# Performance work log

Hardware: AMD Instinct MI355X
Metric: run time of the kernel (lower is better)

The kernel has to match this reference:

```python
import jax, jax.numpy as jnp
import numpy as np
import math

N0 = 50000      # nodes at level 0
E0 = 800000     # edges at level 0 (fixed edge buffer, masked when pooled)
D = 128         # hidden_dim == latent_dim
L = 2           # args.mpl_layers
NB = 2          # args.num_blocks (SAGEConvs per block)
RATIO = 0.5     # args.mpl_ratio
EPS = 1e-12


def setup_inputs() -> dict:
    key = jax.random.key(0)
    ks = jax.random.split(key, 6)
    x = jax.random.normal(ks[0], (N0, D), jnp.float32)
    edge_index = jax.random.randint(ks[1], (2, E0), 0, N0, jnp.int32)
    n_convs = (2 * L + 1) * NB  # down(4) + bottom(2) + up(4) = 10
    Wl = jax.random.normal(ks[2], (n_convs, D, D), jnp.float32) * 0.05
    bl = jax.random.normal(ks[3], (n_convs, D), jnp.float32) * 0.05
    Wr = jax.random.normal(ks[4], (n_convs, D, D), jnp.float32) * 0.05
    pool_p = jax.random.normal(ks[5], (L, D), jnp.float32)
    return {"x": x, "edge_index": edge_index, "Wl": Wl, "bl": bl, "Wr": Wr,
            "pool_p": pool_p}


def _sage(x, src, dst, valid, W_l, b_l, W_r, n):
    """PyG SAGEConv (mean aggr): lin_l(mean_{j->i} x_j) + lin_r(x_i).
    Invalid (masked) edges contribute neither to the sum nor the count."""
    msg = x[src] * valid[:, None]                       # [E, D]
    s = jax.ops.segment_sum(msg, dst, num_segments=n)   # [n, D]
    cnt = jax.ops.segment_sum(valid, dst, num_segments=n)
    mean = s / jnp.maximum(cnt, 1.0)[:, None]
    return mean @ W_l.T + b_l + x @ W_r.T


def _cal_ew(w, src, dst, valid, n):
    """WeightedEdgeConv.cal_ew (no_grad in original)."""
    deg = jax.ops.segment_sum(valid, src, num_segments=n)
    normed = w / jnp.where(deg > 0, deg, 1.0)
    w_send = normed[src] * valid
    aggr_w = jax.ops.segment_sum(w_send, dst, num_segments=n) + EPS
    ec = w_send / aggr_w[dst]
    return jax.lax.stop_gradient(ec), jax.lax.stop_gradient(aggr_w)


def _econv(x, src, dst, ec, n, aggregating=True):
    """WeightedEdgeConv.forward: gather -> scale by edge weight -> scatter-add."""
    if aggregating:
        return jax.ops.segment_sum(x[src] * ec[:, None], dst, num_segments=n)
    return jax.ops.segment_sum(x[dst] * ec[:, None], src, num_segments=n)


def reference(x, edge_index, Wl, bl, Wr, pool_p):
    src, dst = edge_index[0], edge_index[1]
    valid = jnp.ones((E0,), x.dtype)
    n = N0
    conv = 0
    down_outs, down_edges, ecs, perms, sizes = [], [], [], [], []
    w = jnp.ones((N0,), x.dtype)  # b_data.weights (ones by default)

    # ---- down path ----
    for l in range(L):
        for _ in range(NB):
            x = _sage(x, src, dst, valid, Wl[conv], bl[conv], Wr[conv], n)
            conv += 1
        down_outs.append(x)
        down_edges.append((src, dst, valid))
        sizes.append(n)
        ec, w = _cal_ew(w, src, dst, valid, n)
        ecs.append(ec)
        x = _econv(x, src, dst, ec, n, aggregating=True)
        # TopKPooling: score = x.p/||p||, keep top ceil(ratio*n), gate by tanh
        p = pool_p[l]
        score = x @ p / jnp.linalg.norm(p)
        k = int(math.ceil(RATIO * n))
        vals, perm = jax.lax.top_k(score, k)
        x = x[perm] * jnp.tanh(vals)[:, None]
        w = w[perm]
        new_id = jnp.full((n,), -1, jnp.int32).at[perm].set(
            jnp.arange(k, dtype=jnp.int32))
        src2, dst2 = new_id[src], new_id[dst]
        keep = ((src2 >= 0) & (dst2 >= 0)).astype(x.dtype)
        valid = valid * keep
        src = jnp.maximum(src2, 0)
        dst = jnp.maximum(dst2, 0)
        perms.append(perm)
        n = k

    # ---- bottom ----
    for _ in range(NB):
        x = _sage(x, src, dst, valid, Wl[conv], bl[conv], Wr[conv], n)
        conv += 1

    # ---- up path ----
    for i in range(L):
        u = L - 1 - i
        src, dst, valid = down_edges[u]
        n = sizes[u]
        # Unpool: scatter into zeros at kept-node indices
        x = jnp.zeros((n, x.shape[-1]), x.dtype).at[perms[u]].set(x)
        x = _econv(x, src, dst, ecs[u], n, aggregating=False)
        for _ in range(NB):
            x = _sage(x, src, dst, valid, Wl[conv], bl[conv], Wr[conv], n)
            conv += 1
        x = x + down_outs[u]  # skip connection
    return x
```

## Files before the change

### kernel.cpp

```cpp
#include <hip/hip_runtime.h>
#include <stdint.h>

#define DEV __device__ __forceinline__

constexpr int N0 = 50000;
constexpr int E0 = 800000;
constexpr int D  = 128;

typedef __attribute__((ext_vector_type(8))) short bf16x8;
typedef __attribute__((ext_vector_type(4))) float f32x4;

DEV float bf2f(unsigned u) { return __uint_as_float(u << 16); }
DEV unsigned short f2bf(float f) {
  unsigned u = __float_as_uint(f);
  unsigned r = u + 0x7fffu + ((u >> 16) & 1u);
  return (unsigned short)(r >> 16);
}

DEV unsigned wave_incl_scan(unsigned v, int lane) {
  #pragma unroll
  for (int off = 1; off < 64; off <<= 1) {
    unsigned u = __shfl_up(v, (unsigned)off);
    if (lane >= off) v += u;
  }
  return v;
}

__global__ void k_count(const int* __restrict__ src, const int* __restrict__ dst,
                        unsigned* cnt_src, unsigned* cnt_dst,
                        unsigned* __restrict__ rank_src, unsigned* __restrict__ rank_dst) {
  int e = blockIdx.x * blockDim.x + threadIdx.x;
  if (e < E0) {
    rank_src[e] = atomicAdd(&cnt_src[src[e]], 1u);
    rank_dst[e] = atomicAdd(&cnt_dst[dst[e]], 1u);
  }
}

__global__ void k_psum2(const unsigned* __restrict__ in0, const unsigned* __restrict__ in1,
                        int n, unsigned* __restrict__ part) {
  int y = blockIdx.y;
  const unsigned* in = y ? in1 : in0;
  int t = threadIdx.x, lane = t & 63, w = t >> 6;
  int base = blockIdx.x * 1024 + t * 4;
  unsigned s = 0;
  #pragma unroll
  for (int j = 0; j < 4; ++j) { int i = base + j; if (i < n) s += in[i]; }
  #pragma unroll
  for (int off = 32; off >= 1; off >>= 1) s += __shfl_xor(s, off);
  __shared__ unsigned ws[4];
  if (lane == 0) ws[w] = s;
  __syncthreads();
  if (t == 0) part[y * 64 + blockIdx.x] = ws[0] + ws[1] + ws[2] + ws[3];
}

__global__ void k_sapply2(const unsigned* __restrict__ in0, const unsigned* __restrict__ in1,
                          const unsigned* __restrict__ part, int n, int nch,
                          unsigned* __restrict__ out0, unsigned* __restrict__ out1) {
  int y = blockIdx.y;
  const unsigned* in = y ? in1 : in0;
  unsigned* out = y ? out1 : out0;
  int t = threadIdx.x, lane = t & 63, w = t >> 6;
  unsigned c = (lane < (int)blockIdx.x) ? part[y * 64 + lane] : 0u;
  #pragma unroll
  for (int off = 32; off >= 1; off >>= 1) c += __shfl_xor(c, off);
  int base = blockIdx.x * 1024 + t * 4;
  unsigned v[4]; unsigned s = 0;
  #pragma unroll
  for (int j = 0; j < 4; ++j) { int i = base + j; v[j] = (i < n) ? in[i] : 0u; s += v[j]; }
  unsigned incl = wave_incl_scan(s, lane);
  __shared__ unsigned wsum[4], woff[4];
  if (lane == 63) wsum[w] = incl;
  __syncthreads();
  if (t == 0) { unsigned run = 0; for (int j = 0; j < 4; ++j) { woff[j] = run; run += wsum[j]; } }
  __syncthreads();
  unsigned run = c + woff[w] + incl - s;
  #pragma unroll
  for (int j = 0; j < 4; ++j) {
    int i = base + j;
    if (i < n) out[i] = run;
    run += v[j];
  }
  if ((int)blockIdx.x == nch - 1 && t == 0)
    out[n] = c + woff[3] + wsum[3];
}

__global__ void k_fill2(const int* __restrict__ src, const int* __restrict__ dst,
                        const unsigned* __restrict__ rank_src, const unsigned* __restrict__ rank_dst,
                        const unsigned* __restrict__ indptr_src, const unsigned* __restrict__ indptr_dst,
                        int* __restrict__ adj_src, int* __restrict__ adj_dst) {
  int e = blockIdx.x * blockDim.x + threadIdx.x;
  if (e < E0) {
    int s = src[e], d = dst[e];
    adj_dst[indptr_dst[d] + rank_dst[e]] = s;
    adj_src[indptr_src[s] + rank_src[e]] = d;
  }
}

__global__ void k_adj_next2(const int* __restrict__ adjd, const int* __restrict__ adjs,
                            const int* __restrict__ new_id,
                            int* __restrict__ outd, int* __restrict__ outs) {
  int pos = blockIdx.x * blockDim.x + threadIdx.x;
  if (pos < E0) {
    int a = adjd[pos];
    outd[pos] = (a >= 0) ? new_id[a] : -1;
    int b = adjs[pos];
    outs[pos] = (b >= 0) ? new_id[b] : -1;
  }
}

__global__ void k_adj_next(const int* __restrict__ adj_prev, const int* __restrict__ new_id,
                           int* __restrict__ adj_out) {
  int pos = blockIdx.x * blockDim.x + threadIdx.x;
  if (pos < E0) {
    int a = adj_prev[pos];
    adj_out[pos] = (a >= 0) ? new_id[a] : -1;
  }
}

__global__ void k_wt_pk3(const float* __restrict__ Wl, const float* __restrict__ Wr,
                         unsigned short* __restrict__ Bh, unsigned short* __restrict__ Bm,
                         unsigned short* __restrict__ Bl) {
  int idx = blockIdx.x * blockDim.x + threadIdx.x;
  if (idx >= 10 * 8 * 8 * 64) return;
  int l  = idx & 63;
  int ct = (idx >> 6) & 7;
  int ks = (idx >> 9) & 7;
  int c  = idx >> 12;
  int k0 = ks * 32 + (l >> 4) * 8;
  int o  = ct * 16 + (l & 15);
  const float* Wrow = (k0 < 128) ? (Wl + ((size_t)c * 128 + o) * 128 + k0)
                                 : (Wr + ((size_t)c * 128 + o) * 128 + (k0 - 128));
  size_t base = (size_t)idx * 8;
  #pragma unroll
  for (int j = 0; j < 8; ++j) {
    float wv = Wrow[j];
    unsigned short h = f2bf(wv);
    float r1 = wv - bf2f(h);
    unsigned short m = f2bf(r1);
    float r2 = r1 - bf2f(m);
    Bh[base + j] = h;
    Bm[base + j] = m;
    Bl[base + j] = f2bf(r2);
  }
}

template<bool MEAN, bool MASKED, bool ECW>
__global__ void k_gf32(const float* __restrict__ x, const int* __restrict__ adj,
                       const float* __restrict__ ecs, const unsigned* __restrict__ indptr,
                       const int* __restrict__ orig, int n, float* __restrict__ out) {
  int wid = (blockIdx.x * blockDim.x + threadIdx.x) >> 6;
  int lane = threadIdx.x & 63;
  if (wid >= n) return;
  int o = orig ? orig[wid] : wid;
  unsigned s0 = indptr[o], s1 = indptr[o + 1];
  int q = lane >> 4, sl = lane & 15;
  float acc[8];
  #pragma unroll
  for (int k = 0; k < 8; ++k) acc[k] = 0.f;
  float cnt = 0.f;
  for (unsigned idx = s0; idx < s1; idx += 16) {
    #pragma unroll
    for (int j = 0; j < 4; ++j) {
      unsigned e = idx + j * 4 + q;
      if (e < s1) {
        int a = adj[e];
        if (!MASKED || a >= 0) {
          const float4 v0 = *(const float4*)(x + (size_t)a * D + sl * 8);
          const float4 v1 = *(const float4*)(x + (size_t)a * D + sl * 8 + 4);
          if (ECW) {
            float w = ecs[e];
            acc[0] = fmaf(w, v0.x, acc[0]); acc[1] = fmaf(w, v0.y, acc[1]);
            acc[2] = fmaf(w, v0.z, acc[2]); acc[3] = fmaf(w, v0.w, acc[3]);
            acc[4] = fmaf(w, v1.x, acc[4]); acc[5] = fmaf(w, v1.y, acc[5]);
            acc[6] = fmaf(w, v1.z, acc[6]); acc[7] = fmaf(w, v1.w, acc[7]);
          } else {
            acc[0] += v0.x; acc[1] += v0.y; acc[2] += v0.z; acc[3] += v0.w;
            acc[4] += v1.x; acc[5] += v1.y; acc[6] += v1.z; acc[7] += v1.w;
          }
          cnt += 1.f;
        }
      }
    }
  }
  #pragma unroll
  for (int k = 0; k < 8; ++k) {
    acc[k] += __shfl_xor(acc[k], 16);
    acc[k] += __shfl_xor(acc[k], 32);
  }
  if (MEAN) {
    cnt += __shfl_xor(cnt, 16);
    cnt += __shfl_xor(cnt, 32);
    if (!MASKED) cnt = (float)(s1 - s0);
    float inv = 1.0f / fmaxf(cnt, 1.0f);
    #pragma unroll
    for (int k = 0; k < 8; ++k) acc[k] *= inv;
  }
  if (q == 0) {
    *(float4*)(out + (size_t)wid * D + sl * 8)     = make_float4(acc[0], acc[1], acc[2], acc[3]);
    *(float4*)(out + (size_t)wid * D + sl * 8 + 4) = make_float4(acc[4], acc[5], acc[6], acc[7]);
  }
}

template<bool MEAN, bool MASKED, bool ECW>
__global__ void k_gbf(const unsigned* __restrict__ xb, const int* __restrict__ adj,
                      const float* __restrict__ ecs, const unsigned* __restrict__ indptr,
                      const int* __restrict__ orig, int n,
                      float* __restrict__ out, unsigned* __restrict__ outbf) {
  int wid = (blockIdx.x * blockDim.x + threadIdx.x) >> 6;
  int lane = threadIdx.x & 63;
  if (wid >= n) return;
  int o = orig ? orig[wid] : wid;
  unsigned s0 = indptr[o], s1 = indptr[o + 1];
  int q = lane >> 4, sl = lane & 15;
  float acc[8];
  #pragma unroll
  for (int k = 0; k < 8; ++k) acc[k] = 0.f;
  float cnt = 0.f;
  for (unsigned idx = s0; idx < s1; idx += 16) {
    #pragma unroll
    for (int j = 0; j < 4; ++j) {
      unsigned e = idx + j * 4 + q;
      if (e < s1) {
        int a = adj[e];
        if (!MASKED || a >= 0) {
          const uint4 v = *(const uint4*)(xb + (size_t)a * 64 + sl * 4);
          float f0 = bf2f(v.x & 0xffffu), f1 = bf2f(v.x >> 16);
          float f2 = bf2f(v.y & 0xffffu), f3 = bf2f(v.y >> 16);
          float f4 = bf2f(v.z & 0xffffu), f5 = bf2f(v.z >> 16);
          float f6 = bf2f(v.w & 0xffffu), f7 = bf2f(v.w >> 16);
          if (ECW) {
            float w = ecs[e];
            acc[0] = fmaf(w, f0, acc[0]); acc[1] = fmaf(w, f1, acc[1]);
            acc[2] = fmaf(w, f2, acc[2]); acc[3] = fmaf(w, f3, acc[3]);
            acc[4] = fmaf(w, f4, acc[4]); acc[5] = fmaf(w, f5, acc[5]);
            acc[6] = fmaf(w, f6, acc[6]); acc[7] = fmaf(w, f7, acc[7]);
          } else {
            acc[0] += f0; acc[1] += f1; acc[2] += f2; acc[3] += f3;
            acc[4] += f4; acc[5] += f5; acc[6] += f6; acc[7] += f7;
          }
          cnt += 1.f;
        }
      }
    }
  }
  #pragma unroll
  for (int k = 0; k < 8; ++k) {
    acc[k] += __shfl_xor(acc[k], 16);
    acc[k] += __shfl_xor(acc[k], 32);
  }
  if (MEAN) {
    cnt += __shfl_xor(cnt, 16);
    cnt += __shfl_xor(cnt, 32);
    if (!MASKED) cnt = (float)(s1 - s0);
    float inv = 1.0f / fmaxf(cnt, 1.0f);
    #pragma unroll
    for (int k = 0; k < 8; ++k) acc[k] *= inv;
  }
  if (q == 0) {
    *(float4*)(out + (size_t)wid * D + sl * 8)     = make_float4(acc[0], acc[1], acc[2], acc[3]);
    *(float4*)(out + (size_t)wid * D + sl * 8 + 4) = make_float4(acc[4], acc[5], acc[6], acc[7]);
    if (outbf) {
      uint4 p;
      p.x = (unsigned)f2bf(acc[0]) | ((unsigned)f2bf(acc[1]) << 16);
      p.y = (unsigned)f2bf(acc[2]) | ((unsigned)f2bf(acc[3]) << 16);
      p.z = (unsigned)f2bf(acc[4]) | ((unsigned)f2bf(acc[5]) << 16);
      p.w = (unsigned)f2bf(acc[6]) | ((unsigned)f2bf(acc[7]) << 16);
      *(uint4*)(outbf + (size_t)wid * 64 + sl * 4) = p;
    }
  }
}

__launch_bounds__(256)
__global__ void k_gemm_mfma6(const float* __restrict__ mean, const float* __restrict__ xin,
                             const unsigned short* __restrict__ Bh, const unsigned short* __restrict__ Bm,
                             const unsigned short* __restrict__ Bl,
                             const float* __restrict__ bias,
                             float* __restrict__ y, int n) {
  int tid = threadIdx.x;
  int lane = tid & 63, w = tid >> 6;
  int row0 = blockIdx.x * 64 + w * 16;
  int arow = row0 + (lane & 15);
  int kgrp = lane >> 4;
  bool rowok = arow < n;
  f32x4 acc[8];
  #pragma unroll
  for (int ct = 0; ct < 8; ++ct) acc[ct] = f32x4{0.f, 0.f, 0.f, 0.f};

  #pragma unroll
  for (int ks = 0; ks < 8; ++ks) {
    const float* A = (ks < 4) ? mean : xin;
    int kk = (ks & 3) * 32 + kgrp * 8;
    float av[8];
    if (rowok) {
      float4 x0 = *(const float4*)(A + (size_t)arow * D + kk);
      float4 x1 = *(const float4*)(A + (size_t)arow * D + kk + 4);
      av[0] = x0.x; av[1] = x0.y; av[2] = x0.z; av[3] = x0.w;
      av[4] = x1.x; av[5] = x1.y; av[6] = x1.z; av[7] = x1.w;
    } else {
      #pragma unroll
      for (int j = 0; j < 8; ++j) av[j] = 0.f;
    }
    bf16x8 ah, am, al;
    #pragma unroll
    for (int j = 0; j < 8; ++j) {
      unsigned short h = f2bf(av[j]);
      float r1 = av[j] - bf2f(h);
      unsigned short m = f2bf(r1);
      float r2 = r1 - bf2f(m);
      ah[j] = (short)h; am[j] = (short)m; al[j] = (short)f2bf(r2);
    }
    #pragma unroll
    for (int ct = 0; ct < 8; ++ct) {
      size_t boff = (((size_t)ks * 8 + ct) * 64 + lane) * 8;
      bf16x8 bh = *(const bf16x8*)(Bh + boff);
      bf16x8 bm = *(const bf16x8*)(Bm + boff);
      bf16x8 bl = *(const bf16x8*)(Bl + boff);
      acc[ct] = __builtin_amdgcn_mfma_f32_16x16x32_bf16(ah, bh, acc[ct], 0, 0, 0);
      acc[ct] = __builtin_amdgcn_mfma_f32_16x16x32_bf16(ah, bm, acc[ct], 0, 0, 0);
      acc[ct] = __builtin_amdgcn_mfma_f32_16x16x32_bf16(am, bh, acc[ct], 0, 0, 0);
      acc[ct] = __builtin_amdgcn_mfma_f32_16x16x32_bf16(am, bm, acc[ct], 0, 0, 0);
      acc[ct] = __builtin_amdgcn_mfma_f32_16x16x32_bf16(ah, bl, acc[ct], 0, 0, 0);
      acc[ct] = __builtin_amdgcn_mfma_f32_16x16x32_bf16(al, bh, acc[ct], 0, 0, 0);
    }
  }
  int ccol = lane & 15;
  #pragma unroll
  for (int ct = 0; ct < 8; ++ct) {
    int col = ct * 16 + ccol;
    float bb = bias[col];
    #pragma unroll
    for (int r = 0; r < 4; ++r) {
      int row = row0 + kgrp * 4 + r;
      if (row < n) y[(size_t)row * D + col] = acc[ct][r] + bb;
    }
  }
}

__launch_bounds__(256)
__global__ void k_gemm_mfma(const float* __restrict__ mean, const float* __restrict__ xin,
                            const unsigned short* __restrict__ Bhi, const unsigned short* __restrict__ Blo,
                            const float* __restrict__ bias, const float* __restrict__ skip,
                            float* __restrict__ y, unsigned short* __restrict__ ybf, int n) {
  int tid = threadIdx.x;
  int lane = tid & 63, w = tid >> 6;
  int row0 = blockIdx.x * 64 + w * 16;
  int arow = row0 + (lane & 15);
  int kgrp = lane >> 4;
  bool rowok = arow < n;
  f32x4 acc[8];
  #pragma unroll
  for (int ct = 0; ct < 8; ++ct) acc[ct] = f32x4{0.f, 0.f, 0.f, 0.f};

  #pragma unroll
  for (int ks = 0; ks < 8; ++ks) {
    const float* A = (ks < 4) ? mean : xin;
    int kk = (ks & 3) * 32 + kgrp * 8;
    float av[8];
    if (rowok) {
      float4 x0 = *(const float4*)(A + (size_t)arow * D + kk);
      float4 x1 = *(const float4*)(A + (size_t)arow * D + kk + 4);
      av[0] = x0.x; av[1] = x0.y; av[2] = x0.z; av[3] = x0.w;
      av[4] = x1.x; av[5] = x1.y; av[6] = x1.z; av[7] = x1.w;
    } else {
      #pragma unroll
      for (int j = 0; j < 8; ++j) av[j] = 0.f;
    }
    bf16x8 ahi, alo;
    #pragma unroll
    for (int j = 0; j < 8; ++j) {
      unsigned short h = f2bf(av[j]);
      ahi[j] = (short)h;
      alo[j] = (short)f2bf(av[j] - bf2f(h));
    }
    #pragma unroll
    for (int ct = 0; ct < 8; ++ct) {
      size_t boff = (((size_t)ks * 8 + ct) * 64 + lane) * 8;
      bf16x8 bh = *(const bf16x8*)(Bhi + boff);
      bf16x8 bl = *(const bf16x8*)(Blo + boff);
      acc[ct] = __builtin_amdgcn_mfma_f32_16x16x32_bf16(ahi, bh, acc[ct], 0, 0, 0);
      acc[ct] = __builtin_amdgcn_mfma_f32_16x16x32_bf16(alo, bh, acc[ct], 0, 0, 0);
      acc[ct] = __builtin_amdgcn_mfma_f32_16x16x32_bf16(ahi, bl, acc[ct], 0, 0, 0);
    }
  }
  int ccol = lane & 15;
  #pragma unroll
  for (int ct = 0; ct < 8; ++ct) {
    int col = ct * 16 + ccol;
    float bb = bias[col];
    #pragma unroll
    for (int r = 0; r < 4; ++r) {
      int row = row0 + kgrp * 4 + r;
      if (row < n) {
        float v = acc[ct][r] + bb;
        if (skip) v += skip[(size_t)row * D + col];
        y[(size_t)row * D + col] = v;
        if (ybf) ybf[(size_t)row * D + col] = f2bf(v);
      }
    }
  }
}

__global__ void k_deg_mask(const int* __restrict__ adj_src, const unsigned* __restrict__ indptr_src,
                           const int* __restrict__ orig, int n, float* __restrict__ deg) {
  int j = blockIdx.x * blockDim.x + threadIdx.x;
  if (j >= n) return;
  int o = orig ? orig[j] : j;
  unsigned s0 = indptr_src[o], s1 = indptr_src[o + 1];
  float d = 0.f;
  for (unsigned i = s0; i < s1; ++i) d += (adj_src[i] >= 0) ? 1.f : 0.f;
  deg[j] = d;
}

template<bool MASKED>
__global__ void k_ew_dst(const int* __restrict__ adj, const unsigned* __restrict__ indptr,
                         const unsigned* __restrict__ ips,
                         const int* __restrict__ orig, const float* __restrict__ w,
                         const float* __restrict__ deg, int n,
                         float* __restrict__ ws_slot, float* __restrict__ aggrw,
                         float* __restrict__ ec_slot) {
  int j = blockIdx.x * blockDim.x + threadIdx.x;
  if (j >= n) return;
  int o = orig ? orig[j] : j;
  unsigned s0 = indptr[o], s1 = indptr[o + 1];
  float s = 1e-12f;
  for (unsigned pos = s0; pos < s1; ++pos) {
    int a = adj[pos];
    float ws = 0.f;
    if (!MASKED || a >= 0) {
      float d = deg ? deg[a] : (float)(ips[a + 1] - ips[a]);
      ws = (w ? w[a] : 1.0f) / (d > 0.f ? d : 1.0f);
    }
    ws_slot[pos] = ws;
    s += ws;
  }
  aggrw[j] = s;
  float inv = 1.0f / s;
  for (unsigned pos = s0; pos < s1; ++pos) ec_slot[pos] = ws_slot[pos] * inv;
}

template<bool MASKED>
__global__ void k_ew_src(const int* __restrict__ adj_src, const unsigned* __restrict__ indptr_src,
                         const int* __restrict__ orig, const float* __restrict__ w,
                         const float* __restrict__ deg, const float* __restrict__ aggrw, int n,
                         float* __restrict__ ec_slot) {
  int j = blockIdx.x * blockDim.x + threadIdx.x;
  if (j >= n) return;
  int o = orig ? orig[j] : j;
  unsigned s0 = indptr_src[o], s1 = indptr_src[o + 1];
  float d = deg ? deg[j] : (float)(s1 - s0);
  float wn = (w ? w[j] : 1.0f) / (d > 0.f ? d : 1.0f);
  for (unsigned pos = s0; pos < s1; ++pos) {
    int a = adj_src[pos];
    ec_slot[pos] = (!MASKED || a >= 0) ? (wn / aggrw[a]) : 0.f;
  }
}

DEV unsigned mono_key(float f) {
  unsigned u = __float_as_uint(f);
  return (u & 0x80000000u) ? ~u : (u | 0x80000000u);
}

__global__ void k_score(const float* __restrict__ x, const float* __restrict__ p,
                        int n, float* __restrict__ score, unsigned* __restrict__ keys,
                        unsigned* bins, unsigned* state, int k) {
  if (blockIdx.x == 0) {
    int t = threadIdx.x;
    if (t < 256) bins[t] = 0u;
    if (t == 0) { state[0] = 0u; state[1] = (unsigned)k; }
  }
  int wid = (blockIdx.x * blockDim.x + threadIdx.x) >> 6;
  int lane = threadIdx.x & 63;
  if (wid >= n) return;
  float p0 = p[lane * 2], p1 = p[lane * 2 + 1];
  const float2 xv = *(const float2*)(x + (size_t)wid * D + lane * 2);
  float partial = xv.x * p0 + xv.y * p1;
  float pn = p0 * p0 + p1 * p1;
  #pragma unroll
  for (int off = 32; off >= 1; off >>= 1) {
    partial += __shfl_xor(partial, off);
    pn += __shfl_xor(pn, off);
  }
  if (lane == 0) {
    float sc = partial * (1.0f / sqrtf(pn));
    score[wid] = sc;
    keys[wid] = mono_key(sc);
  }
}

__global__ void k_hist(const unsigned* __restrict__ keys, int n, const unsigned* __restrict__ state,
                       unsigned* __restrict__ bins, int byte) {
  __shared__ unsigned lb[256];
  for (int i = threadIdx.x; i < 256; i += blockDim.x) lb[i] = 0u;
  __syncthreads();
  unsigned prefix = state[0];
  unsigned mask = (byte == 3) ? 0u : (0xFFFFFFFFu << ((byte + 1) * 8));
  for (int i = blockIdx.x * blockDim.x + threadIdx.x; i < n; i += gridDim.x * blockDim.x) {
    unsigned key = keys[i];
    if ((key & mask) == (prefix & mask))
      atomicAdd(&lb[(key >> (byte * 8)) & 255], 1u);
  }
  __syncthreads();
  for (int i = threadIdx.x; i < 256; i += blockDim.x)
    if (lb[i]) atomicAdd(&bins[i], lb[i]);
}

__global__ void k_pick(unsigned* bins, unsigned* state, int byte) {
  if (threadIdx.x == 0) {
    unsigned r = state[1];
    int b;
    for (b = 255; b > 0; --b) {
      unsigned c = bins[b];
      if (c >= r) break;
      r -= c;
    }
    state[0] |= ((unsigned)b) << (byte * 8);
    state[1] = r;
  }
  __syncthreads();
  for (int i = threadIdx.x; i < 256; i += blockDim.x) bins[i] = 0u;
}

__global__ void k_flags(const unsigned* __restrict__ keys, const unsigned* __restrict__ state,
                        int n, uint2* __restrict__ part) {
  int t = threadIdx.x, lane = t & 63, w = t >> 6;
  int base = blockIdx.x * 1024 + t * 4;
  unsigned T = state[0];
  unsigned cnt = 0;
  #pragma unroll
  for (int j = 0; j < 4; ++j) {
    int i = base + j;
    if (i < n) {
      unsigned key = keys[i];
      cnt += (key > T ? 1u : 0u) + ((key == T ? 1u : 0u) << 16);
    }
  }
  #pragma unroll
  for (int off = 32; off >= 1; off >>= 1) cnt += __shfl_xor(cnt, off);
  __shared__ unsigned ws[4];
  if (lane == 0) ws[w] = cnt;
  __syncthreads();
  if (t == 0) {
    unsigned s = ws[0] + ws[1] + ws[2] + ws[3];
    part[blockIdx.x] = make_uint2(s & 0xffffu, s >> 16);
  }
}

__global__ void k_pack2(const unsigned* __restrict__ keys, const unsigned* __restrict__ state,
                        const uint2* __restrict__ part, const float* __restrict__ aggrw,
                        const int* __restrict__ orig, int n,
                        int* __restrict__ perm, int* __restrict__ new_id,
                        float* __restrict__ w_next, int* __restrict__ orig_next) {
  int t = threadIdx.x, lane = t & 63, w = t >> 6;
  int base = blockIdx.x * 1024 + t * 4;
  unsigned T = state[0], r = state[1];
  unsigned co = 0;
  if (lane < (int)blockIdx.x) {
    uint2 pp = part[lane];
    co = pp.x | (pp.y << 16);
  }
  #pragma unroll
  for (int off = 32; off >= 1; off >>= 1) co += __shfl_xor(co, off);
  unsigned f[4];
  unsigned cnt = 0;
  #pragma unroll
  for (int j = 0; j < 4; ++j) {
    int i = base + j;
    unsigned key = (i < n) ? keys[i] : 0u;
    unsigned gt = (i < n && key > T) ? 1u : 0u;
    unsigned eq = (i < n && key == T) ? 1u : 0u;
    f[j] = gt | (eq << 1);
    cnt += gt + (eq << 16);
  }
  unsigned incl = wave_incl_scan(cnt, lane);
  __shared__ unsigned wsum[4], woff[4];
  if (lane == 63) wsum[w] = incl;
  __syncthreads();
  if (t == 0) { unsigned run = 0; for (int j = 0; j < 4; ++j) { woff[j] = run; run += wsum[j]; } }
  __syncthreads();
  unsigned before = woff[w] + incl - cnt;
  unsigned gt_b = (co & 0xffffu) + (before & 0xffffu);
  unsigned eq_b = (co >> 16) + (before >> 16);
  #pragma unroll
  for (int j = 0; j < 4; ++j) {
    int i = base + j;
    if (i >= n) break;
    unsigned gt = f[j] & 1u, eq = (f[j] >> 1) & 1u;
    bool sel = gt || (eq && eq_b < r);
    if (sel) {
      int pos = (int)(gt_b + (eq_b < r ? eq_b : r));
      perm[pos] = i;
      new_id[i] = pos;
      w_next[pos] = aggrw[i];
      orig_next[pos] = orig ? orig[i] : i;
    } else {
      new_id[i] = -1;
    }
    gt_b += gt; eq_b += eq;
  }
}

__global__ void k_gate(const float* __restrict__ xin, const int* __restrict__ perm,
                       const float* __restrict__ score, int k, float* __restrict__ xout,
                       unsigned* __restrict__ outbf) {
  int wid = (blockIdx.x * blockDim.x + threadIdx.x) >> 6;
  int lane = threadIdx.x & 63;
  if (wid >= k) return;
  int j = perm[wid];
  float g = tanhf(score[j]);
  float2 v = *(const float2*)(xin + (size_t)j * D + lane * 2);
  v.x *= g; v.y *= g;
  *(float2*)(xout + (size_t)wid * D + lane * 2) = v;
  if (outbf) {
    unsigned p = (unsigned)f2bf(v.x) | ((unsigned)f2bf(v.y) << 16);
    outbf[(size_t)wid * 64 + lane] = p;
  }
}

__global__ void k_unpool_bf(const float* __restrict__ xin, const int* __restrict__ new_id,
                            int n, unsigned* __restrict__ outbf) {
  int wid = (blockIdx.x * blockDim.x + threadIdx.x) >> 6;
  int lane = threadIdx.x & 63;
  if (wid >= n) return;
  int j = new_id[wid];
  unsigned pk = 0u;
  if (j >= 0) {
    float2 v = *(const float2*)(xin + (size_t)j * D + lane * 2);
    pk = (unsigned)f2bf(v.x) | ((unsigned)f2bf(v.y) << 16);
  }
  outbf[(size_t)wid * 64 + lane] = pk;
}

extern "C" void kernel_launch(void* const* d_in, const int* in_sizes, int n_in,
                              void* d_out, int out_size, void* d_ws, size_t ws_size,
                              hipStream_t stream) {
  const float* x_in   = (const float*)d_in[0];
  const int*   ei     = (const int*)d_in[1];
  const int*   src0   = ei;
  const int*   dst0   = ei + E0;
  const float* Wl     = (const float*)d_in[2];
  const float* bl     = (const float*)d_in[3];
  const float* Wr     = (const float*)d_in[4];
  const float* pool_p = (const float*)d_in[5];
  float* out = (float*)d_out;

  const int n0 = N0, k0 = 25000, n1 = 25000, k1 = 12500, n2 = 12500;
  const int NCH0 = (N0 + 1023) / 1024;

  char* ws = (char*)d_ws;
  size_t off = 0;
  auto alloc = [&](size_t bytes) -> char* {
    char* p = ws + off;
    off += (bytes + 255) & ~(size_t)255;
    return p;
  };
  const size_t NBY = (size_t)N0 * D * 4;
  float* B0    = (float*)alloc(NBY);
  float* B1    = (float*)alloc(NBY);
  float* B2    = (float*)alloc(NBY);
  float* down0 = (float*)alloc(NBY);
  float* down1 = (float*)alloc(NBY / 2);
  unsigned* MA = (unsigned*)alloc((size_t)N0 * D * 2);
  unsigned* MB = (unsigned*)alloc((size_t)N0 * D * 2);
  int* adj0_dst = (int*)alloc(E0 * 4);
  int* adj0_src = (int*)alloc(E0 * 4);
  int* adj1_dst = (int*)alloc(E0 * 4);
  int* adj1_src = (int*)alloc(E0 * 4);
  float* ec0_src = (float*)alloc(E0 * 4);
  float* ec1_src = (float*)alloc(E0 * 4);
  float* ec_dst  = (float*)alloc(E0 * 4);
  float* ws_slot = (float*)alloc(E0 * 4);
  int* adj2_dst  = (int*)ws_slot;
  unsigned* rank_src = (unsigned*)alloc(E0 * 4);
  unsigned* rank_dst = (unsigned*)alloc(E0 * 4);
  unsigned* indptr_dst = (unsigned*)alloc((N0 + 1) * 4);
  unsigned* indptr_src = (unsigned*)alloc((N0 + 1) * 4);
  unsigned* cnt_src = (unsigned*)alloc(N0 * 4);
  unsigned* cnt_dst = (unsigned*)alloc(N0 * 4);
  float* deg   = (float*)alloc(N0 * 4);
  float* aggrw = (float*)alloc(N0 * 4);
  float* w1 = (float*)alloc(n1 * 4);
  float* w2 = (float*)alloc(n2 * 4);
  float* score = (float*)alloc(N0 * 4);
  unsigned* keys = (unsigned*)alloc(N0 * 4);
  int* perm0 = (int*)alloc(k0 * 4);
  int* perm1 = (int*)alloc(k1 * 4);
  int* orig1 = (int*)alloc(k0 * 4);
  int* orig2 = (int*)alloc(k1 * 4);
  int* new_id0 = (int*)alloc(N0 * 4);
  int* new_id1 = (int*)alloc(N0 * 4);
  unsigned* bins  = (unsigned*)alloc(256 * 4);
  unsigned* state = (unsigned*)alloc(8);
  unsigned* spart = (unsigned*)alloc(128 * 4);
  uint2* ppart = (uint2*)alloc(64 * 8);
  unsigned short* Bh = (unsigned short*)alloc((size_t)10 * 32768 * 2);
  unsigned short* Bm = (unsigned short*)alloc((size_t)10 * 32768 * 2);
  unsigned short* Bl = (unsigned short*)alloc((size_t)10 * 32768 * 2);

  const int EG = (E0 + 255) / 256;

  hipMemsetAsync(cnt_src, 0, N0 * 4, stream);
  hipMemsetAsync(cnt_dst, 0, N0 * 4, stream);
  k_count<<<EG, 256, 0, stream>>>(src0, dst0, cnt_src, cnt_dst, rank_src, rank_dst);
  k_psum2<<<dim3(NCH0, 2), 256, 0, stream>>>(cnt_src, cnt_dst, N0, spart);
  k_sapply2<<<dim3(NCH0, 2), 256, 0, stream>>>(cnt_src, cnt_dst, spart, N0, NCH0,
                                               indptr_src, indptr_dst);
  k_fill2<<<EG, 256, 0, stream>>>(src0, dst0, rank_src, rank_dst, indptr_src, indptr_dst,
                                  adj0_src, adj0_dst);
  k_wt_pk3<<<(10 * 8 * 8 * 64 + 255) / 256, 256, 0, stream>>>(Wl, Wr, Bh, Bm, Bl);

  auto gemm6 = [&](const float* meanb, const float* xin, float* yout, int n, int cidx) {
    size_t o = (size_t)cidx * 32768;
    k_gemm_mfma6<<<(n + 63) / 64, 256, 0, stream>>>(meanb, xin, Bh + o, Bm + o, Bl + o,
                                                    bl + cidx * 128, yout, n);
  };
  auto gemm_mx = [&](const float* meanb, const float* xin, float* yout, unsigned short* ybf,
                     const float* skip, int n, int cidx) {
    size_t o = (size_t)cidx * 32768;
    k_gemm_mfma<<<(n + 63) / 64, 256, 0, stream>>>(meanb, xin, Bh + o, Bm + o,
                                                   bl + cidx * 128, skip, yout, ybf, n);
  };

  auto pool_sel = [&](const float* xpool, int n, int kk, int level, const int* orig,
                      int* perm, int* nid, float* w_next, int* orig_next,
                      float* xout, unsigned* xout_bf) {
    int nch = (n + 1023) / 1024;
    k_score<<<(n + 3) / 4, 256, 0, stream>>>(xpool, pool_p + level * D, n, score, keys,
                                             bins, state, kk);
    for (int byte = 3; byte >= 0; --byte) {
      k_hist<<<256, 256, 0, stream>>>(keys, n, state, bins, byte);
      k_pick<<<1, 256, 0, stream>>>(bins, state, byte);
    }
    k_flags<<<nch, 256, 0, stream>>>(keys, state, n, ppart);
    k_pack2<<<nch, 256, 0, stream>>>(keys, state, ppart, aggrw, orig, n, perm, nid, w_next, orig_next);
    k_gate<<<(kk + 3) / 4, 256, 0, stream>>>(xpool, perm, score, kk, xout, xout_bf);
  };

  const int G0 = (n0 + 3) / 4, G1 = (n1 + 3) / 4, G2 = (n2 + 3) / 4;

  k_gf32<true, false, false><<<G0, 256, 0, stream>>>(x_in, adj0_dst, nullptr, indptr_dst, nullptr, n0, B1);
  gemm6(B1, x_in, B2, n0, 0);
  k_gf32<true, false, false><<<G0, 256, 0, stream>>>(B2, adj0_dst, nullptr, indptr_dst, nullptr, n0, B1);
  gemm6(B1, B2, down0, n0, 1);
  k_ew_dst<false><<<(n0 + 255) / 256, 256, 0, stream>>>(adj0_dst, indptr_dst, indptr_src, nullptr,
                                                        nullptr, nullptr, n0, ws_slot, aggrw, ec_dst);
  k_ew_src<false><<<(n0 + 255) / 256, 256, 0, stream>>>(adj0_src, indptr_src, nullptr, nullptr,
                                                        nullptr, aggrw, n0, ec0_src);
  k_gf32<false, false, true><<<G0, 256, 0, stream>>>(down0, adj0_dst, ec_dst, indptr_dst, nullptr, n0, B1);
  pool_sel(B1, n0, k0, 0, nullptr, perm0, new_id0, w1, orig1, B2, nullptr);
  k_adj_next2<<<EG, 256, 0, stream>>>(adj0_dst, adj0_src, new_id0, adj1_dst, adj1_src);

  k_gf32<true, true, false><<<G1, 256, 0, stream>>>(B2, adj1_dst, nullptr, indptr_dst, orig1, n1, B1);
  gemm6(B1, B2, B0, n1, 2);
  k_gf32<true, true, false><<<G1, 256, 0, stream>>>(B0, adj1_dst, nullptr, indptr_dst, orig1, n1, B1);
  gemm6(B1, B0, down1, n1, 3);
  k_deg_mask<<<(n1 + 255) / 256, 256, 0, stream>>>(adj1_src, indptr_src, orig1, n1, deg);
  k_ew_dst<true><<<(n1 + 255) / 256, 256, 0, stream>>>(adj1_dst, indptr_dst, nullptr, orig1, w1,
                                                       deg, n1, ws_slot, aggrw, ec_dst);
  k_ew_src<true><<<(n1 + 255) / 256, 256, 0, stream>>>(adj1_src, indptr_src, orig1, w1, deg, aggrw,
                                                       n1, ec1_src);
  k_gf32<false, true, true><<<G1, 256, 0, stream>>>(down1, adj1_dst, ec_dst, indptr_dst, orig1, n1, B1);
  pool_sel(B1, n1, k1, 1, orig1, perm1, new_id1, w2, orig2, B2, MA);
  k_adj_next<<<EG, 256, 0, stream>>>(adj1_dst, new_id1, adj2_dst);

  k_gbf<true, true, false><<<G2, 256, 0, stream>>>(MA, adj2_dst, nullptr, indptr_dst, orig2, n2, B1, nullptr);
  gemm_mx(B1, B2, B0, (unsigned short*)MB, nullptr, n2, 4);
  k_gbf<true, true, false><<<G2, 256, 0, stream>>>(MB, adj2_dst, nullptr, indptr_dst, orig2, n2, B1, nullptr);
  gemm_mx(B1, B0, B2, nullptr, nullptr, n2, 5);

  k_unpool_bf<<<G1, 256, 0, stream>>>(B2, new_id1, n1, MA);
  k_gbf<false, true, true><<<G1, 256, 0, stream>>>(MA, adj1_src, ec1_src, indptr_src, orig1, n1, B1, MB);
  k_gbf<true, true, false><<<G1, 256, 0, stream>>>(MB, adj1_dst, nullptr, indptr_dst, orig1, n1, B0, nullptr);
  gemm_mx(B0, B1, B2, (unsigned short*)MA, nullptr, n1, 6);
  k_gbf<true, true, false><<<G1, 256, 0, stream>>>(MA, adj1_dst, nullptr, indptr_dst, orig1, n1, B0, nullptr);
  gemm_mx(B0, B2, B1, nullptr, down1, n1, 7);

  k_unpool_bf<<<G0, 256, 0, stream>>>(B1, new_id0, n0, MA);
  k_gbf<false, false, true><<<G0, 256, 0, stream>>>(MA, adj0_src, ec0_src, indptr_src, nullptr, n0, B2, MB);
  k_gbf<true, false, false><<<G0, 256, 0, stream>>>(MB, adj0_dst, nullptr, indptr_dst, nullptr, n0, B1, nullptr);
  gemm_mx(B1, B2, B0, (unsigned short*)MA, nullptr, n0, 8);
  k_gbf<true, false, false><<<G0, 256, 0, stream>>>(MA, adj0_dst, nullptr, indptr_dst, nullptr, n0, B1, nullptr);
  gemm_mx(B1, B0, out, nullptr, down0, n0, 9);
}
```

Measured before the change: 1.090 ms.

## Fuse pool scoring into aggregation, merge hist/pick, skip unpool via remapped adjacency

Computes the pooling score and radix key inside the edge-weighted aggregation kernel, so a separate score pass over x is no longer needed. It merges the histogram and pick kernels using a last-block-done atomic counter. It also removes the unpool kernels: the un-aggregating gather reads the compact pooled bf16 output directly, using a source adjacency remapped to pooled ids, with masked entries standing in for zeroed rows. The goal is fewer launches and less memory traffic, at the cost of an extra adjacency buffer and a correctness dependence on the remap and masking.

```diff
diff --git a/kernel.cpp b/kernel.cpp
--- a/kernel.cpp
+++ b/kernel.cpp
@@ -24,6 +24,11 @@
     if (lane >= off) v += u;
   }
   return v;
+}
+
+DEV unsigned mono_key(float f) {
+  unsigned u = __float_as_uint(f);
+  return (u & 0x80000000u) ? ~u : (u | 0x80000000u);
 }
 
 __global__ void k_count(const int* __restrict__ src, const int* __restrict__ dst,
@@ -105,15 +110,6 @@
     outd[pos] = (a >= 0) ? new_id[a] : -1;
     int b = adjs[pos];
     outs[pos] = (b >= 0) ? new_id[b] : -1;
-  }
-}
-
-__global__ void k_adj_next(const int* __restrict__ adj_prev, const int* __restrict__ new_id,
-                           int* __restrict__ adj_out) {
-  int pos = blockIdx.x * blockDim.x + threadIdx.x;
-  if (pos < E0) {
-    int a = adj_prev[pos];
-    adj_out[pos] = (a >= 0) ? new_id[a] : -1;
   }
 }
 
@@ -144,10 +140,17 @@
   }
 }
 
-template<bool MEAN, bool MASKED, bool ECW>
+template<bool MEAN, bool MASKED, bool ECW, bool SCORE>
 __global__ void k_gf32(const float* __restrict__ x, const int* __restrict__ adj,
                        const float* __restrict__ ecs, const unsigned* __restrict__ indptr,
-                       const int* __restrict__ orig, int n, float* __restrict__ out) {
+                       const int* __restrict__ orig, int n, float* __restrict__ out,
+                       const float* __restrict__ p, float* __restrict__ score,
+                       unsigned* __restrict__ keys, unsigned* bins, unsigned* state, int kk) {
+  if (SCORE && blockIdx.x == 0) {
+    int t = threadIdx.x;
+    if (t < 256) bins[t] = 0u;
+    if (t == 0) { state[0] = 0u; state[1] = (unsigned)kk; state[2] = 0u; }
+  }
   int wid = (blockIdx.x * blockDim.x + threadIdx.x) >> 6;
   int lane = threadIdx.x & 63;
   if (wid >= n) return;
@@ -198,6 +201,25 @@
   if (q == 0) {
     *(float4*)(out + (size_t)wid * D + sl * 8)     = make_float4(acc[0], acc[1], acc[2], acc[3]);
     *(float4*)(out + (size_t)wid * D + sl * 8 + 4) = make_float4(acc[4], acc[5], acc[6], acc[7]);
+    if (SCORE) {
+      float partial = 0.f, pn = 0.f;
+      #pragma unroll
+      for (int k = 0; k < 8; ++k) {
+        float pv = p[sl * 8 + k];
+        partial = fmaf(acc[k], pv, partial);
+        pn = fmaf(pv, pv, pn);
+      }
+      #pragma unroll
+      for (int off = 8; off >= 1; off >>= 1) {
+        partial += __shfl_xor(partial, off);
+        pn += __shfl_xor(pn, off);
+      }
+      if (sl == 0) {
+        float sc = partial * (1.0f / sqrtf(pn));
+        score[wid] = sc;
+        keys[wid] = mono_key(sc);
+      }
+    }
   }
 }
 
@@ -455,41 +477,10 @@
   }
 }
 
-DEV unsigned mono_key(float f) {
-  unsigned u = __float_as_uint(f);
-  return (u & 0x80000000u) ? ~u : (u | 0x80000000u);
-}
-
-__global__ void k_score(const float* __restrict__ x, const float* __restrict__ p,
-                        int n, float* __restrict__ score, unsigned* __restrict__ keys,
-                        unsigned* bins, unsigned* state, int k) {
-  if (blockIdx.x == 0) {
-    int t = threadIdx.x;
-    if (t < 256) bins[t] = 0u;
-    if (t == 0) { state[0] = 0u; state[1] = (unsigned)k; }
-  }
-  int wid = (blockIdx.x * blockDim.x + threadIdx.x) >> 6;
-  int lane = threadIdx.x & 63;
-  if (wid >= n) return;
-  float p0 = p[lane * 2], p1 = p[lane * 2 + 1];
-  const float2 xv = *(const float2*)(x + (size_t)wid * D + lane * 2);
-  float partial = xv.x * p0 + xv.y * p1;
-  float pn = p0 * p0 + p1 * p1;
-  #pragma unroll
-  for (int off = 32; off >= 1; off >>= 1) {
-    partial += __shfl_xor(partial, off);
-    pn += __shfl_xor(pn, off);
-  }
-  if (lane == 0) {
-    float sc = partial * (1.0f / sqrtf(pn));
-    score[wid] = sc;
-    keys[wid] = mono_key(sc);
-  }
-}
-
-__global__ void k_hist(const unsigned* __restrict__ keys, int n, const unsigned* __restrict__ state,
-                       unsigned* __restrict__ bins, int byte) {
+__global__ void k_histpick(const unsigned* __restrict__ keys, int n,
+                           unsigned* state, unsigned* bins, int byte) {
   __shared__ unsigned lb[256];
+  __shared__ int last;
   for (int i = threadIdx.x; i < 256; i += blockDim.x) lb[i] = 0u;
   __syncthreads();
   unsigned prefix = state[0];
@@ -502,22 +493,29 @@
   __syncthreads();
   for (int i = threadIdx.x; i < 256; i += blockDim.x)
     if (lb[i]) atomicAdd(&bins[i], lb[i]);
-}
-
-__global__ void k_pick(unsigned* bins, unsigned* state, int byte) {
+  __threadfence();
   if (threadIdx.x == 0) {
-    unsigned r = state[1];
-    int b;
-    for (b = 255; b > 0; --b) {
-      unsigned c = bins[b];
-      if (c >= r) break;
-      r -= c;
-    }
-    state[0] |= ((unsigned)b) << (byte * 8);
-    state[1] = r;
-  }
-  __syncthreads();
-  for (int i = threadIdx.x; i < 256; i += blockDim.x) bins[i] = 0u;
+    unsigned t = atomicAdd(&state[2], 1u);
+    last = (t == gridDim.x - 1) ? 1 : 0;
+  }
+  __syncthreads();
+  if (last) {
+    __threadfence();
+    if (threadIdx.x == 0) {
+      unsigned r = state[1];
+      int b;
+      for (b = 255; b > 0; --b) {
+        unsigned c = bins[b];
+        if (c >= r) break;
+        r -= c;
+      }
+      state[0] = prefix | (((unsigned)b) << (byte * 8));
+      state[1] = r;
+      state[2] = 0u;
+    }
+    __syncthreads();
+    for (int i = threadIdx.x; i < 256; i += blockDim.x) bins[i] = 0u;
+  }
 }
 
 __global__ void k_flags(const unsigned* __restrict__ keys, const unsigned* __restrict__ state,
@@ -614,20 +612,6 @@
     unsigned p = (unsigned)f2bf(v.x) | ((unsigned)f2bf(v.y) << 16);
     outbf[(size_t)wid * 64 + lane] = p;
   }
-}
-
-__global__ void k_unpool_bf(const float* __restrict__ xin, const int* __restrict__ new_id,
-                            int n, unsigned* __restrict__ outbf) {
-  int wid = (blockIdx.x * blockDim.x + threadIdx.x) >> 6;
-  int lane = threadIdx.x & 63;
-  if (wid >= n) return;
-  int j = new_id[wid];
-  unsigned pk = 0u;
-  if (j >= 0) {
-    float2 v = *(const float2*)(xin + (size_t)j * D + lane * 2);
-    pk = (unsigned)f2bf(v.x) | ((unsigned)f2bf(v.y) << 16);
-  }
-  outbf[(size_t)wid * 64 + lane] = pk;
 }
 
 extern "C" void kernel_launch(void* const* d_in, const int* in_sizes, int n_in,
@@ -665,6 +649,7 @@
   int* adj0_src = (int*)alloc(E0 * 4);
   int* adj1_dst = (int*)alloc(E0 * 4);
   int* adj1_src = (int*)alloc(E0 * 4);
+  int* adj2_src = (int*)alloc(E0 * 4);
   float* ec0_src = (float*)alloc(E0 * 4);
   float* ec1_src = (float*)alloc(E0 * 4);
   float* ec_dst  = (float*)alloc(E0 * 4);
@@ -689,7 +674,7 @@
   int* new_id0 = (int*)alloc(N0 * 4);
   int* new_id1 = (int*)alloc(N0 * 4);
   unsigned* bins  = (unsigned*)alloc(256 * 4);
-  unsigned* state = (unsigned*)alloc(8);
+  unsigned* state = (unsigned*)alloc(16);
   unsigned* spart = (unsigned*)alloc(128 * 4);
   uint2* ppart = (uint2*)alloc(64 * 8);
   unsigned short* Bh = (unsigned short*)alloc((size_t)10 * 32768 * 2);
@@ -720,62 +705,62 @@
                                                    bl + cidx * 128, skip, yout, ybf, n);
   };
 
-  auto pool_sel = [&](const float* xpool, int n, int kk, int level, const int* orig,
+  auto pool_sel = [&](const float* xpool, int n, int kk, const int* orig,
                       int* perm, int* nid, float* w_next, int* orig_next,
                       float* xout, unsigned* xout_bf) {
     int nch = (n + 1023) / 1024;
-    k_score<<<(n + 3) / 4, 256, 0, stream>>>(xpool, pool_p + level * D, n, score, keys,
-                                             bins, state, kk);
-    for (int byte = 3; byte >= 0; --byte) {
-      k_hist<<<256, 256, 0, stream>>>(keys, n, state, bins, byte);
-      k_pick<<<1, 256, 0, stream>>>(bins, state, byte);
-    }
+    for (int byte = 3; byte >= 0; --byte)
+      k_histpick<<<256, 256, 0, stream>>>(keys, n, state, bins, byte);
     k_flags<<<nch, 256, 0, stream>>>(keys, state, n, ppart);
     k_pack2<<<nch, 256, 0, stream>>>(keys, state, ppart, aggrw, orig, n, perm, nid, w_next, orig_next);
-    k_gate<<<(kk + 3) / 4, 256, 0, stream>>>(xpool, perm, score, kk, xout, xout_bf);
+    k_gate<<<((kk + 3) / 4), 256, 0, stream>>>(xpool, perm, score, kk, xout, xout_bf);
   };
 
   const int G0 = (n0 + 3) / 4, G1 = (n1 + 3) / 4, G2 = (n2 + 3) / 4;
 
-  k_gf32<true, false, false><<<G0, 256, 0, stream>>>(x_in, adj0_dst, nullptr, indptr_dst, nullptr, n0, B1);
+  k_gf32<true, false, false, false><<<G0, 256, 0, stream>>>(x_in, adj0_dst, nullptr, indptr_dst,
+      nullptr, n0, B1, nullptr, nullptr, nullptr, nullptr, nullptr, 0);
   gemm6(B1, x_in, B2, n0, 0);
-  k_gf32<true, false, false><<<G0, 256, 0, stream>>>(B2, adj0_dst, nullptr, indptr_dst, nullptr, n0, B1);
+  k_gf32<true, false, false, false><<<G0, 256, 0, stream>>>(B2, adj0_dst, nullptr, indptr_dst,
+      nullptr, n0, B1, nullptr, nullptr, nullptr, nullptr, nullptr, 0);
   gemm6(B1, B2, down0, n0, 1);
   k_ew_dst<false><<<(n0 + 255) / 256, 256, 0, stream>>>(adj0_dst, indptr_dst, indptr_src, nullptr,
                                                         nullptr, nullptr, n0, ws_slot, aggrw, ec_dst);
   k_ew_src<false><<<(n0 + 255) / 256, 256, 0, stream>>>(adj0_src, indptr_src, nullptr, nullptr,
                                                         nullptr, aggrw, n0, ec0_src);
-  k_gf32<false, false, true><<<G0, 256, 0, stream>>>(down0, adj0_dst, ec_dst, indptr_dst, nullptr, n0, B1);
-  pool_sel(B1, n0, k0, 0, nullptr, perm0, new_id0, w1, orig1, B2, nullptr);
+  k_gf32<false, false, true, true><<<G0, 256, 0, stream>>>(down0, adj0_dst, ec_dst, indptr_dst,
+      nullptr, n0, B1, pool_p, score, keys, bins, state, k0);
+  pool_sel(B1, n0, k0, nullptr, perm0, new_id0, w1, orig1, B2, nullptr);
   k_adj_next2<<<EG, 256, 0, stream>>>(adj0_dst, adj0_src, new_id0, adj1_dst, adj1_src);
 
-  k_gf32<true, true, false><<<G1, 256, 0, stream>>>(B2, adj1_dst, nullptr, indptr_dst, orig1, n1, B1);
+  k_gf32<true, true, false, false><<<G1, 256, 0, stream>>>(B2, adj1_dst, nullptr, indptr_dst,
+      orig1, n1, B1, nullptr, nullptr, nullptr, nullptr, nullptr, 0);
   gemm6(B1, B2, B0, n1, 2);
-  k_gf32<true, true, false><<<G1, 256, 0, stream>>>(B0, adj1_dst, nullptr, indptr_dst, orig1, n1, B1);
+  k_gf32<true, true, false, false><<<G1, 256, 0, stream>>>(B0, adj1_dst, nullptr, indptr_dst,
+      orig1, n1, B1, nullptr, nullptr, nullptr, nullptr, nullptr, 0);
   gemm6(B1, B0, down1, n1, 3);
   k_deg_mask<<<(n1 + 255) / 256, 256, 0, stream>>>(adj1_src, indptr_src, orig1, n1, deg);
   k_ew_dst<true><<<(n1 + 255) / 256, 256, 0, stream>>>(adj1_dst, indptr_dst, nullptr, orig1, w1,
                                                        deg, n1, ws_slot, aggrw, ec_dst);
   k_ew_src<true><<<(n1 + 255) / 256, 256, 0, stream>>>(adj1_src, indptr_src, orig1, w1, deg, aggrw,
                                                        n1, ec1_src);
-  k_gf32<false, true, true><<<G1, 256, 0, stream>>>(down1, adj1_dst, ec_dst, indptr_dst, orig1, n1, B1);
-  pool_sel(B1, n1, k1, 1, orig1, perm1, new_id1, w2, orig2, B2, MA);
-  k_adj_next<<<EG, 256, 0, stream>>>(adj1_dst, new_id1, adj2_dst);
+  k_gf32<false, true, true, true><<<G1, 256, 0, stream>>>(down1, adj1_dst, ec_dst, indptr_dst,
+      orig1, n1, B1, pool_p + D, score, keys, bins, state, k1);
+  pool_sel(B1, n1, k1, orig1, perm1, new_id1, w2, orig2, B2, MA);
+  k_adj_next2<<<EG, 256, 0, stream>>>(adj1_dst, adj1_src, new_id1, adj2_dst, adj2_src);
 
   k_gbf<true, true, false><<<G2, 256, 0, stream>>>(MA, adj2_dst, nullptr, indptr_dst, orig2, n2, B1, nullptr);
   gemm_mx(B1, B2, B0, (unsigned short*)MB, nullptr, n2, 4);
   k_gbf<true, true, false><<<G2, 256, 0, stream>>>(MB, adj2_dst, nullptr, indptr_dst, orig2, n2, B1, nullptr);
-  gemm_mx(B1, B0, B2, nullptr, nullptr, n2, 5);
-
-  k_unpool_bf<<<G1, 256, 0, stream>>>(B2, new_id1, n1, MA);
-  k_gbf<false, true, true><<<G1, 256, 0, stream>>>(MA, adj1_src, ec1_src, indptr_src, orig1, n1, B1, MB);
+  gemm_mx(B1, B0, B2, (unsigned short*)MA, nullptr, n2, 5);
+
+  k_gbf<false, true, true><<<G1, 256, 0, stream>>>(MA, adj2_src, ec1_src, indptr_src, orig1, n1, B1, MB);
   k_gbf<true, true, false><<<G1, 256, 0, stream>>>(MB, adj1_dst, nullptr, indptr_dst, orig1, n1, B0, nullptr);
   gemm_mx(B0, B1, B2, (unsigned short*)MA, nullptr, n1, 6);
   k_gbf<true, true, false><<<G1, 256, 0, stream>>>(MA, adj1_dst, nullptr, indptr_dst, orig1, n1, B0, nullptr);
-  gemm_mx(B0, B2, B1, nullptr, down1, n1, 7);
-
-  k_unpool_bf<<<G0, 256, 0, stream>>>(B1, new_id0, n0, MA);
-  k_gbf<false, false, true><<<G0, 256, 0, stream>>>(MA, adj0_src, ec0_src, indptr_src, nullptr, n0, B2, MB);
+  gemm_mx(B0, B2, B1, (unsigned short*)MA, down1, n1, 7);
+
+  k_gbf<false, true, true><<<G0, 256, 0, stream>>>(MA, adj1_src, ec0_src, indptr_src, nullptr, n0, B2, MB);
   k_gbf<true, false, false><<<G0, 256, 0, stream>>>(MB, adj0_dst, nullptr, indptr_dst, nullptr, n0, B1, nullptr);
   gemm_mx(B1, B2, B0, (unsigned short*)MA, nullptr, n0, 8);
   k_gbf<true, false, false><<<G0, 256, 0, stream>>>(MA, adj0_dst, nullptr, indptr_dst, nullptr, n0, B1, nullptr);
```

Result: slower. 1.193 ms (+9.4%).
